# Kernel optimization log

Hardware: AMD Instinct MI355X
Metric: run time of the kernel (lower is better)

Reference implementation:

```python
import jax, jax.numpy as jnp
import numpy as np

NUM_HEADS = 16

def setup_inputs() -> dict:
    key = jax.random.key(0)
    k1, k2, k3 = jax.random.split(key, 3)
    B, N, C = 2, 2048, 1024
    x = jax.random.normal(k1, (B, N, C), dtype=jnp.float32)
    # Dense layers: qkv (C -> 3C, no bias), proj (C -> C, with bias)
    w_qkv = jax.random.normal(k2, (C, 3 * C), dtype=jnp.float32) * (C ** -0.5)
    w_proj = jax.random.normal(k3, (C, C), dtype=jnp.float32) * (C ** -0.5)
    b_proj = jnp.zeros((C,), dtype=jnp.float32)
    return {"x": x, "w_qkv": w_qkv, "w_proj": w_proj, "b_proj": b_proj}

def reference(x, w_qkv, w_proj, b_proj):
    B, N, C = x.shape
    H = NUM_HEADS
    Dh = C // H
    scale = Dh ** -0.5
    qkv = x @ w_qkv                                   # [B,N,3C]
    qkv = qkv.reshape(B, N, 3, H, Dh)
    qkv = jnp.transpose(qkv, (2, 0, 3, 1, 4))         # [3,B,H,N,Dh]
    q, k, v = qkv[0], qkv[1], qkv[2]
    attn = jnp.einsum('bhnd,bhmd->bhnm', q, k) * scale  # [B,H,N,N]
    attn = jax.nn.softmax(attn, axis=-1)
    out = jnp.einsum('bhnm,bhmd->bhnd', attn, v)        # [B,H,N,Dh]
    out = jnp.transpose(out, (0, 2, 1, 3)).reshape(B, N, C)
    return out @ w_proj + b_proj
```

## Files before the change

kernel.cpp:

```cpp
#include <hip/hip_runtime.h>
#include <stdint.h>


typedef unsigned short u16;
typedef uint32_t u32;
typedef __bf16 bf16x8 __attribute__((ext_vector_type(8)));
typedef unsigned short u16x8 __attribute__((ext_vector_type(8)));
typedef float f32x4 __attribute__((ext_vector_type(4)));
typedef float f32x16 __attribute__((ext_vector_type(16)));
typedef uint32_t u32x2v __attribute__((ext_vector_type(2)));
typedef uint32_t u32x4v __attribute__((ext_vector_type(4)));

#define DEV static __device__ __forceinline__

DEV u16 f2bf(float f) {
    uint32_t u = __float_as_uint(f);
    u += 0x7fffu + ((u >> 16) & 1u);
    return (u16)(u >> 16);
}

DEV u32 cvtpk(float lo, float hi_) {
    u32 r;
    asm("v_cvt_pk_bf16_f32 %0, %1, %2" : "=v"(r) : "v"(lo), "v"(hi_));
    return r;
}
DEV void plswap(u32& x, u32& y) {
    asm("v_permlane32_swap_b32 %0, %1" : "+v"(x), "+v"(y));
}
DEV float exp2f_fast(float x) {
    float r;
    asm("v_exp_f32 %0, %1" : "=v"(r) : "v"(x));
    return r;
}

DEV void gload_lds16(const void* g, void* l) {
    __builtin_amdgcn_global_load_lds(
        (const __attribute__((address_space(1))) uint32_t*)g,
        (__attribute__((address_space(3))) uint32_t*)l, 16, 0, 0);
}

#define WAIT_VM(N) asm volatile("s_waitcnt vmcnt(" #N ")" ::: "memory")
#define RAW_BAR() __builtin_amdgcn_s_barrier()
#define SCHED_PIN() __builtin_amdgcn_sched_barrier(0)

DEV bf16x8 swz_load16(const u16* base, int row, int kbyte) {
    int off = (row * 128 + kbyte) ^ ((row & 7) << 4);
    return *reinterpret_cast<const bf16x8*>(reinterpret_cast<const char*>(base) + off);
}

__global__ __launch_bounds__(256) void prep_kernel(
    const float* __restrict__ x, u16* __restrict__ xb,
    const float* __restrict__ wq, u16* __restrict__ wqt,
    const float* __restrict__ wp, u16* __restrict__ wpt) {
    __shared__ float T[32][33];
    int b = blockIdx.x, tid = threadIdx.x;
    if (b < 2048) {
        int t = b * 256 + tid;
        const float4* p = reinterpret_cast<const float4*>(x) + (size_t)t * 2;
        float4 a = p[0], c = p[1];
        u16x8 o;
        o[0] = f2bf(a.x); o[1] = f2bf(a.y); o[2] = f2bf(a.z); o[3] = f2bf(a.w);
        o[4] = f2bf(c.x); o[5] = f2bf(c.y); o[6] = f2bf(c.z); o[7] = f2bf(c.w);
        reinterpret_cast<u16x8*>(xb)[t] = o;
        return;
    }
    const float* in;
    u16* out;
    int bx, by, R = 1024, Cc;
    if (b < 5120) {
        int idx = b - 2048;
        bx = idx % 96; by = idx / 96; Cc = 3072; in = wq; out = wqt;
    } else {
        int idx = b - 5120;
        bx = idx % 32; by = idx / 32; Cc = 1024; in = wp; out = wpt;
    }
    int tx = tid & 31, ty = tid >> 5;
    int xcol = bx * 32 + tx;
    int y0 = by * 32;
#pragma unroll
    for (int i = 0; i < 4; i++) {
        int y = y0 + ty + i * 8;
        T[ty + i * 8][tx] = in[(size_t)y * Cc + xcol];
    }
    __syncthreads();
    int xo = y0 + tx;
    int yo0 = bx * 32;
#pragma unroll
    for (int i = 0; i < 4; i++) {
        int yo = yo0 + ty + i * 8;
        out[(size_t)yo * R + xo] = f2bf(T[tx][ty + i * 8]);
    }
}

__global__ __launch_bounds__(256, 2) void gemm1_kernel(
    const u16* __restrict__ A, const u16* __restrict__ Bt,
    u16* __restrict__ o_q, u16* __restrict__ o_k, u16* __restrict__ o_vt) {
    __shared__ __align__(16) u16 Al[8192];
    __shared__ __align__(16) u16 Bl[8192];
    int tid = threadIdx.x;
    int p = blockIdx.x;
    int xcd = p & 7, q = p >> 3;
    int bm = xcd * 4 + (q & 3), bn = q >> 2;
    int lane = tid & 63, w = tid >> 6;
    int wr = w >> 1, wc = w & 1;
    int l15 = lane & 15, lhi = lane >> 4;

    f32x4 acc[4][4];
#pragma unroll
    for (int i = 0; i < 4; i++)
#pragma unroll
        for (int j = 0; j < 4; j++) acc[i][j] = (f32x4){0.f, 0.f, 0.f, 0.f};

    for (int kt = 0; kt < 16; ++kt) {
#pragma unroll
        for (int i = 0; i < 4; i++) {
            int lin = w * 4096 + i * 1024 + lane * 16;
            int row = lin >> 7;
            int src = (lin & 127) ^ ((row & 7) << 4);
            gload_lds16((const char*)A + (size_t)(bm * 128 + row) * 2048 + (size_t)kt * 128 + src,
                        (char*)Al + lin);
            gload_lds16((const char*)Bt + (size_t)(bn * 128 + row) * 2048 + (size_t)kt * 128 + src,
                        (char*)Bl + lin);
        }
        __syncthreads();
#pragma unroll
        for (int ks = 0; ks < 2; ++ks) {
            bf16x8 af[4], bfr[4];
#pragma unroll
            for (int mi = 0; mi < 4; ++mi) af[mi] = swz_load16(Al, wr * 64 + mi * 16 + l15, ks * 64 + lhi * 16);
#pragma unroll
            for (int ni = 0; ni < 4; ++ni) bfr[ni] = swz_load16(Bl, wc * 64 + ni * 16 + l15, ks * 64 + lhi * 16);
            __builtin_amdgcn_s_setprio(1);
#pragma unroll
            for (int mi = 0; mi < 4; ++mi)
#pragma unroll
                for (int ni = 0; ni < 4; ++ni)
                    acc[mi][ni] = __builtin_amdgcn_mfma_f32_16x16x32_bf16(af[mi], bfr[ni], acc[mi][ni], 0, 0, 0);
            __builtin_amdgcn_s_setprio(0);
        }
        __syncthreads();
    }

    int row0 = bm * 128 + wr * 64, col0 = bn * 128 + wc * 64;
#pragma unroll
    for (int mi = 0; mi < 4; mi++)
#pragma unroll
        for (int ni = 0; ni < 4; ni++) {
            int col = col0 + ni * 16 + l15;
            int sel = col >> 10, cc = col & 1023;
            int h = cc >> 6, d = cc & 63;
            int r0 = row0 + mi * 16 + lhi * 4;
            int b = r0 >> 11, n0 = r0 & 2047;
            if (sel == 2) {
                u32x2v pk2 = {cvtpk(acc[mi][ni][0], acc[mi][ni][1]),
                              cvtpk(acc[mi][ni][2], acc[mi][ni][3])};
                *reinterpret_cast<u32x2v*>(o_vt + ((size_t)(b * 16 + h) * 64 + d) * 2048 + n0) = pk2;
            } else {
                size_t base = (((size_t)(b * 16 + h)) * 2048 + n0) * 64 + d;
#pragma unroll
                for (int j = 0; j < 4; j++) {
                    float v = acc[mi][ni][j];
                    if (sel == 0) o_q[base + (size_t)j * 64] = f2bf(v * 0.18033688f);
                    else o_k[base + (size_t)j * 64] = f2bf(v);
                }
            }
        }
}

__global__ __launch_bounds__(256, 4) void gemm2_kernel(
    const u16* __restrict__ A, const u16* __restrict__ Bt,
    float* __restrict__ o_f, const float* __restrict__ bias) {
    __shared__ __align__(16) u16 Al[4096];
    __shared__ __align__(16) u16 Bl[4096];
    int tid = threadIdx.x;
    int p = blockIdx.x;
    int xcd = p & 7, q = p >> 3;
    int bm = xcd * 8 + (q & 7), bn = q >> 3;
    int lane = tid & 63, w = tid >> 6;
    int wr = w >> 1, wc = w & 1;
    int l15 = lane & 15, lhi = lane >> 4;

    f32x4 acc[2][2];
#pragma unroll
    for (int i = 0; i < 2; i++)
#pragma unroll
        for (int j = 0; j < 2; j++) acc[i][j] = (f32x4){0.f, 0.f, 0.f, 0.f};

    for (int kt = 0; kt < 16; ++kt) {
#pragma unroll
        for (int i = 0; i < 2; i++) {
            int lin = tid * 16 + i * 4096;
            int row = lin >> 7;
            int src = (lin & 127) ^ ((row & 7) << 4);
            gload_lds16((const char*)A + (size_t)(bm * 64 + row) * 2048 + (size_t)kt * 128 + src,
                        (char*)Al + lin);
            gload_lds16((const char*)Bt + (size_t)(bn * 64 + row) * 2048 + (size_t)kt * 128 + src,
                        (char*)Bl + lin);
        }
        __syncthreads();
#pragma unroll
        for (int ks = 0; ks < 2; ++ks) {
            bf16x8 af[2], bfr[2];
#pragma unroll
            for (int mi = 0; mi < 2; ++mi) af[mi] = swz_load16(Al, wr * 32 + mi * 16 + l15, ks * 64 + lhi * 16);
#pragma unroll
            for (int ni = 0; ni < 2; ++ni) bfr[ni] = swz_load16(Bl, wc * 32 + ni * 16 + l15, ks * 64 + lhi * 16);
            __builtin_amdgcn_s_setprio(1);
#pragma unroll
            for (int mi = 0; mi < 2; ++mi)
#pragma unroll
                for (int ni = 0; ni < 2; ++ni)
                    acc[mi][ni] = __builtin_amdgcn_mfma_f32_16x16x32_bf16(af[mi], bfr[ni], acc[mi][ni], 0, 0, 0);
            __builtin_amdgcn_s_setprio(0);
        }
        __syncthreads();
    }

    int row0 = bm * 64 + wr * 32, col0 = bn * 64 + wc * 32;
#pragma unroll
    for (int mi = 0; mi < 2; mi++)
#pragma unroll
        for (int ni = 0; ni < 2; ni++) {
            int col = col0 + ni * 16 + l15;
            float bb = bias[col];
#pragma unroll
            for (int j = 0; j < 4; j++) {
                int r = row0 + mi * 16 + lhi * 4 + j;
                o_f[(size_t)r * 1024 + col] = acc[mi][ni][j] + bb;
            }
        }
}

__global__ __launch_bounds__(512, 4) void flash6_kernel(
    const u16* __restrict__ qg, const u16* __restrict__ kg, const u16* __restrict__ vtg,
    u16* __restrict__ o) {
    __shared__ __align__(16) char smem[65536];

    int tid = threadIdx.x, lane = tid & 63, w = tid >> 6;
    int wg = w & 3, g = w >> 2;
    int l31 = lane & 31, hi = lane >> 5;
    int p = blockIdx.y * 16 + blockIdx.x;
    int bh = p & 31, qt = p >> 5;
    int q0 = qt * 128 + wg * 32;

#define KL(gg, bb) (smem + ((gg) * 2 + (bb)) * 8192)
#define VL(gg, bb) (smem + 32768 + ((gg) * 2 + (bb)) * 8192)

    const u16* qp = qg + ((size_t)bh * 2048 + q0 + l31) * 64 + hi * 8;
    bf16x8 qf[4];
#pragma unroll
    for (int ds = 0; ds < 4; ds++) qf[ds] = *reinterpret_cast<const bf16x8*>(qp + ds * 16);

    const char* kbg = (const char*)(kg + (size_t)bh * 2048 * 64) + (size_t)g * 16 * 8192;
    const char* vbg = (const char*)(vtg + (size_t)bh * 64 * 2048) + (size_t)g * 2048;

    int srow = lane >> 1, sinner = (lane & 1) * 16;
    int fbase = l31 * 32 + hi * 16;

#define STAGE(bb, tt)                                                                     \
    {                                                                                     \
        _Pragma("unroll") for (int i = 0; i < 2; i++) {                                   \
            gload_lds16(kbg + (size_t)(tt) * 8192 + (i * 32 + srow) * 128 + wg * 32 + sinner, \
                        KL(g, bb) + wg * 2048 + i * 1024 + lane * 16);                    \
            gload_lds16(vbg + (size_t)(i * 32 + srow) * 4096 + (size_t)(tt) * 128 + wg * 32 + sinner, \
                        VL(g, bb) + wg * 2048 + i * 1024 + lane * 16);                    \
        }                                                                                 \
    }

    f32x16 fzero;
#pragma unroll
    for (int r = 0; r < 16; r++) fzero[r] = 0.f;
    f32x16 accO[2], accL;
#pragma unroll
    for (int db = 0; db < 2; db++) accO[db] = fzero;
    accL = fzero;
    u16x8 ou;
#pragma unroll
    for (int j = 0; j < 8; j++) ou[j] = 0x3F80;
    bf16x8 ones = __builtin_bit_cast(bf16x8, ou);

    STAGE(0, 0);

    for (int pp = 0; pp < 16; ++pp) {
        int c = pp & 1;
        if (pp < 15) {
            STAGE(c ^ 1, pp + 1);
            WAIT_VM(4);
        } else {
            WAIT_VM(0);
        }
        RAW_BAR();
        SCHED_PIN();

        bf16x8 ka[2][4];
#pragma unroll
        for (int kvb = 0; kvb < 2; kvb++)
#pragma unroll
            for (int ds = 0; ds < 4; ds++)
                ka[kvb][ds] = *reinterpret_cast<const bf16x8*>(KL(g, c) + ds * 2048 + kvb * 1024 + fbase);
        f32x16 s[2];
        __builtin_amdgcn_s_setprio(1);
#pragma unroll
        for (int kvb = 0; kvb < 2; kvb++) {
            s[kvb] = __builtin_amdgcn_mfma_f32_32x32x16_bf16(ka[kvb][0], qf[0], fzero, 0, 0, 0);
#pragma unroll
            for (int ds = 1; ds < 4; ds++)
                s[kvb] = __builtin_amdgcn_mfma_f32_32x32x16_bf16(ka[kvb][ds], qf[ds], s[kvb], 0, 0, 0);
        }
        __builtin_amdgcn_s_setprio(0);

#pragma unroll
        for (int kvb = 0; kvb < 2; kvb++)
#pragma unroll
            for (int r = 0; r < 16; r++) s[kvb][r] = exp2f_fast(s[kvb][r]);

        bf16x8 pb[4];
#pragma unroll
        for (int kvb = 0; kvb < 2; kvb++) {
            u32 x0 = cvtpk(s[kvb][0], s[kvb][1]), y0 = cvtpk(s[kvb][4], s[kvb][5]);
            u32 x1 = cvtpk(s[kvb][2], s[kvb][3]), y1 = cvtpk(s[kvb][6], s[kvb][7]);
            u32 x2 = cvtpk(s[kvb][8], s[kvb][9]), y2 = cvtpk(s[kvb][12], s[kvb][13]);
            u32 x3 = cvtpk(s[kvb][10], s[kvb][11]), y3 = cvtpk(s[kvb][14], s[kvb][15]);
            plswap(x0, y0); plswap(x1, y1); plswap(x2, y2); plswap(x3, y3);
            u32x4v plo = {x0, x1, y0, y1};
            u32x4v phi = {x2, x3, y2, y3};
            pb[2 * kvb] = __builtin_bit_cast(bf16x8, plo);
            pb[2 * kvb + 1] = __builtin_bit_cast(bf16x8, phi);
        }

        bf16x8 va[2][4];
#pragma unroll
        for (int db = 0; db < 2; db++)
#pragma unroll
            for (int ks = 0; ks < 4; ks++)
                va[db][ks] = *reinterpret_cast<const bf16x8*>(VL(g, c) + ks * 2048 + db * 1024 + fbase);
        __builtin_amdgcn_s_setprio(1);
#pragma unroll
        for (int ks = 0; ks < 4; ks++) {
            accO[0] = __builtin_amdgcn_mfma_f32_32x32x16_bf16(va[0][ks], pb[ks], accO[0], 0, 0, 0);
            accO[1] = __builtin_amdgcn_mfma_f32_32x32x16_bf16(va[1][ks], pb[ks], accO[1], 0, 0, 0);
            accL = __builtin_amdgcn_mfma_f32_32x32x16_bf16(ones, pb[ks], accL, 0, 0, 0);
        }
        __builtin_amdgcn_s_setprio(0);

        RAW_BAR();
    }
#undef STAGE

    float lsum = accL[0];

    float* mbuf = (float*)smem;
    int base = (wg * 64 + lane) * 36;
    if (g == 1) {
#pragma unroll
        for (int db = 0; db < 2; db++)
#pragma unroll
            for (int q4 = 0; q4 < 4; q4++) {
                f32x4 v4 = {accO[db][q4 * 4 + 0], accO[db][q4 * 4 + 1],
                            accO[db][q4 * 4 + 2], accO[db][q4 * 4 + 3]};
                *reinterpret_cast<f32x4*>(mbuf + base + db * 16 + q4 * 4) = v4;
            }
        mbuf[base + 32] = lsum;
    }
    __syncthreads();
    if (g == 0) {
        float lsum2 = mbuf[base + 32];
        float inv = 1.f / (lsum + lsum2);
        int b = bh >> 4, h = bh & 15;
        u16* ob = o + ((size_t)(b * 2048 + q0 + l31)) * 1024 + h * 64;
#pragma unroll
        for (int db = 0; db < 2; db++) {
            f32x4 m4[4];
#pragma unroll
            for (int q4 = 0; q4 < 4; q4++)
                m4[q4] = *reinterpret_cast<const f32x4*>(mbuf + base + db * 16 + q4 * 4);
#pragma unroll
            for (int i = 0; i < 8; i++) {
                int r = 2 * i;
                int d = (r & 3) + 8 * (r >> 2) + 4 * hi + 32 * db;
                float lo = (accO[db][r] + m4[r >> 2][r & 3]) * inv;
                float hi_ = (accO[db][r + 1] + m4[(r + 1) >> 2][(r + 1) & 3]) * inv;
                *reinterpret_cast<u32*>(ob + d) = cvtpk(lo, hi_);
            }
        }
    }
#undef KL
#undef VL
}


extern "C" void kernel_launch(void* const* d_in, const int* in_sizes, int n_in,
                              void* d_out, int out_size, void* d_ws, size_t ws_size,
                              hipStream_t stream) {
    (void)in_sizes; (void)n_in; (void)out_size; (void)ws_size;
    const float* x = (const float*)d_in[0];
    const float* w_qkv = (const float*)d_in[1];
    const float* w_proj = (const float*)d_in[2];
    const float* b_proj = (const float*)d_in[3];
    float* out = (float*)d_out;
    char* ws = (char*)d_ws;

    u16* xb   = (u16*)(ws + 0);
    u16* wqt  = (u16*)(ws + 8388608);
    u16* wpt  = (u16*)(ws + 14680064);
    u16* qws  = (u16*)(ws + 16777216);
    u16* kws  = (u16*)(ws + 25165824);
    u16* vtws = (u16*)(ws + 41943040);
    u16* attn = (u16*)(ws + 50331648);

    prep_kernel<<<6144, 256, 0, stream>>>(x, xb, w_qkv, wqt, w_proj, wpt);
    gemm1_kernel<<<768, 256, 0, stream>>>(xb, wqt, qws, kws, vtws);
    flash6_kernel<<<dim3(16, 32), 512, 0, stream>>>(qws, kws, vtws, attn);
    gemm2_kernel<<<1024, 256, 0, stream>>>(attn, wpt, out, b_proj);
}
```

Baseline: 98.49 us.

## Restructure QKV GEMM into 256x256 tiles with double-buffered pipelined LDS loads

Rewrites the QKV projection GEMM to use 256x256 output tiles per 512-thread block with a 128KB double-buffered LDS. Each K-step is split into four phases, and the next tiles' async global-to-LDS loads are interleaved with MFMA work under explicit vmcnt waits and raw barriers. The goal is to hide global load latency and raise arithmetic intensity per block. In exchange the grid shrinks from 768 to 192 blocks, so fewer than one block runs per CU and occupancy drops to one block per CU. The hand-tuned wait counts must also match the issue order exactly, which is fragile.

```diff
diff --git a/kernel.cpp b/kernel.cpp
--- a/kernel.cpp
+++ b/kernel.cpp
@@ -92,64 +92,89 @@
     }
 }
 
-__global__ __launch_bounds__(256, 2) void gemm1_kernel(
+__global__ __launch_bounds__(512, 1) void gemm1_kernel(
     const u16* __restrict__ A, const u16* __restrict__ Bt,
     u16* __restrict__ o_q, u16* __restrict__ o_k, u16* __restrict__ o_vt) {
-    __shared__ __align__(16) u16 Al[8192];
-    __shared__ __align__(16) u16 Bl[8192];
+    __shared__ __align__(16) char sm[131072];
     int tid = threadIdx.x;
     int p = blockIdx.x;
     int xcd = p & 7, q = p >> 3;
-    int bm = xcd * 4 + (q & 3), bn = q >> 2;
+    int bm = xcd * 2 + (q & 1), bn = q >> 1;
     int lane = tid & 63, w = tid >> 6;
-    int wr = w >> 1, wc = w & 1;
+    int wr = w >> 2, wc = w & 3;
     int l15 = lane & 15, lhi = lane >> 4;
 
-    f32x4 acc[4][4];
-#pragma unroll
-    for (int i = 0; i < 4; i++)
+    f32x4 acc[8][4];
+#pragma unroll
+    for (int i = 0; i < 8; i++)
 #pragma unroll
         for (int j = 0; j < 4; j++) acc[i][j] = (f32x4){0.f, 0.f, 0.f, 0.f};
 
-    for (int kt = 0; kt < 16; ++kt) {
-#pragma unroll
-        for (int i = 0; i < 4; i++) {
-            int lin = w * 4096 + i * 1024 + lane * 16;
-            int row = lin >> 7;
-            int src = (lin & 127) ^ ((row & 7) << 4);
-            gload_lds16((const char*)A + (size_t)(bm * 128 + row) * 2048 + (size_t)kt * 128 + src,
-                        (char*)Al + lin);
-            gload_lds16((const char*)Bt + (size_t)(bn * 128 + row) * 2048 + (size_t)kt * 128 + src,
-                        (char*)Bl + lin);
-        }
-        __syncthreads();
-#pragma unroll
-        for (int ks = 0; ks < 2; ++ks) {
-            bf16x8 af[4], bfr[4];
-#pragma unroll
-            for (int mi = 0; mi < 4; ++mi) af[mi] = swz_load16(Al, wr * 64 + mi * 16 + l15, ks * 64 + lhi * 16);
-#pragma unroll
-            for (int ni = 0; ni < 4; ++ni) bfr[ni] = swz_load16(Bl, wc * 64 + ni * 16 + l15, ks * 64 + lhi * 16);
-            __builtin_amdgcn_s_setprio(1);
-#pragma unroll
-            for (int mi = 0; mi < 4; ++mi)
-#pragma unroll
-                for (int ni = 0; ni < 4; ++ni)
-                    acc[mi][ni] = __builtin_amdgcn_mfma_f32_16x16x32_bf16(af[mi], bfr[ni], acc[mi][ni], 0, 0, 0);
-            __builtin_amdgcn_s_setprio(0);
-        }
-        __syncthreads();
-    }
-
-    int row0 = bm * 128 + wr * 64, col0 = bn * 128 + wc * 64;
-#pragma unroll
-    for (int mi = 0; mi < 4; mi++)
+#define ST(kt_, isB_, h_)                                                                    \
+    {                                                                                        \
+        _Pragma("unroll") for (int i_ = 0; i_ < 2; i_++) {                                   \
+            int lin = (h_) * 16384 + tid * 16 + i_ * 8192;                                   \
+            int row = lin >> 7;                                                              \
+            int src = (lin & 127) ^ ((row & 7) << 4);                                        \
+            const char* gp = (isB_) ? (const char*)Bt + (size_t)(bn * 256 + row) * 2048      \
+                                    : (const char*)A + (size_t)(bm * 256 + row) * 2048;      \
+            gload_lds16(gp + (size_t)(kt_)*128 + src,                                        \
+                        sm + ((kt_) & 1) * 65536 + (isB_) * 32768 + lin);                    \
+        }                                                                                    \
+    }
+
+#define PHASE(mih, nih, STAGES, WAITS)                                                       \
+    {                                                                                        \
+        const u16* smA_ = (const u16*)(sm + cslot * 65536);                                  \
+        const u16* smB_ = (const u16*)(sm + cslot * 65536 + 32768);                          \
+        bf16x8 af[4][2], bfr[2][2];                                                          \
+        _Pragma("unroll") for (int m2 = 0; m2 < 4; m2++)                                     \
+            _Pragma("unroll") for (int ks = 0; ks < 2; ks++)                                 \
+                af[m2][ks] = swz_load16(smA_, ((mih)*4 + m2) * 32 + wr * 16 + l15,           \
+                                        ks * 64 + lhi * 16);                                 \
+        _Pragma("unroll") for (int n2 = 0; n2 < 2; n2++)                                     \
+            _Pragma("unroll") for (int ks = 0; ks < 2; ks++)                                 \
+                bfr[n2][ks] = swz_load16(smB_, ((nih)*2 + n2) * 64 + wc * 16 + l15,          \
+                                         ks * 64 + lhi * 16);                                \
+        STAGES;                                                                              \
+        RAW_BAR();                                                                           \
+        __builtin_amdgcn_s_setprio(1);                                                       \
+        _Pragma("unroll") for (int m2 = 0; m2 < 4; m2++)                                     \
+            _Pragma("unroll") for (int n2 = 0; n2 < 2; n2++)                                 \
+                _Pragma("unroll") for (int ks = 0; ks < 2; ks++)                             \
+                    acc[(mih)*4 + m2][(nih)*2 + n2] = __builtin_amdgcn_mfma_f32_16x16x32_bf16( \
+                        af[m2][ks], bfr[n2][ks], acc[(mih)*4 + m2][(nih)*2 + n2], 0, 0, 0);  \
+        __builtin_amdgcn_s_setprio(0);                                                       \
+        WAITS;                                                                               \
+        RAW_BAR();                                                                           \
+    }
+
+    ST(0, 0, 0); ST(0, 0, 1); ST(0, 1, 0); ST(0, 1, 1);
+    ST(1, 0, 0); ST(1, 0, 1); ST(1, 1, 0); ST(1, 1, 1);
+    WAIT_VM(8);
+    RAW_BAR();
+
+    for (int j = 0; j < 16; ++j) {
+        int cslot = j & 1;
+        PHASE(0, 0, { if (j >= 1 && j <= 14) ST(j + 1, 0, 1); }, {});
+        PHASE(1, 0, { if (j >= 1 && j <= 14) ST(j + 1, 1, 1); },
+              { if (j == 15) { WAIT_VM(0); } else if (j >= 1) { WAIT_VM(6); } });
+        PHASE(0, 1, { if (j <= 13) ST(j + 2, 1, 0); }, {});
+        PHASE(1, 1, { if (j <= 13) ST(j + 2, 0, 0); },
+              { if (j == 0) { WAIT_VM(4); } else if (j == 14) { WAIT_VM(2); }
+                else if (j <= 13) { WAIT_VM(6); } });
+    }
+#undef PHASE
+#undef ST
+
+#pragma unroll
+    for (int mi = 0; mi < 8; mi++)
 #pragma unroll
         for (int ni = 0; ni < 4; ni++) {
-            int col = col0 + ni * 16 + l15;
+            int col = bn * 256 + ni * 64 + wc * 16 + l15;
             int sel = col >> 10, cc = col & 1023;
             int h = cc >> 6, d = cc & 63;
-            int r0 = row0 + mi * 16 + lhi * 4;
+            int r0 = bm * 256 + mi * 32 + wr * 16 + lhi * 4;
             int b = r0 >> 11, n0 = r0 & 2047;
             if (sel == 2) {
                 u32x2v pk2 = {cvtpk(acc[mi][ni][0], acc[mi][ni][1]),
@@ -158,10 +183,10 @@
             } else {
                 size_t base = (((size_t)(b * 16 + h)) * 2048 + n0) * 64 + d;
 #pragma unroll
-                for (int j = 0; j < 4; j++) {
-                    float v = acc[mi][ni][j];
-                    if (sel == 0) o_q[base + (size_t)j * 64] = f2bf(v * 0.18033688f);
-                    else o_k[base + (size_t)j * 64] = f2bf(v);
+                for (int jj = 0; jj < 4; jj++) {
+                    float v = acc[mi][ni][jj];
+                    if (sel == 0) o_q[base + (size_t)jj * 64] = f2bf(v * 0.18033688f);
+                    else o_k[base + (size_t)jj * 64] = f2bf(v);
                 }
             }
         }
@@ -409,7 +434,7 @@
     u16* attn = (u16*)(ws + 50331648);
 
     prep_kernel<<<6144, 256, 0, stream>>>(x, xb, w_qkv, wqt, w_proj, wpt);
-    gemm1_kernel<<<768, 256, 0, stream>>>(xb, wqt, qws, kws, vtws);
+    gemm1_kernel<<<192, 512, 0, stream>>>(xb, wqt, qws, kws, vtws);
     flash6_kernel<<<dim3(16, 32), 512, 0, stream>>>(qws, kws, vtws, attn);
     gemm2_kernel<<<1024, 256, 0, stream>>>(attn, wpt, out, b_proj);
 }
```

Result: slower. 113.4 us (+15.1%).
